# Kernel optimization log

Hardware: AMD Instinct MI355X
Metric: run time of the kernel (lower is better)

## Reference

```python
import jax, jax.numpy as jnp
import numpy as np

# Poincare ball hyperbolic multi-head attention (hypll-style HMultiheadAttention)
C = 1.0          # ball curvature
SQRT_C = 1.0
EPS = 1e-7
B, S, E, H = 4, 1024, 512, 8
HD = E // H      # head_dim = 64


def _project_to_ball(u, scale=0.5):
    n = jnp.linalg.norm(u, axis=-1, keepdims=True)
    return u * (scale / (1.0 + n))  # guarantees ||x|| < scale < 1/sqrt(C)


def h_linear(x, z, r):
    """Poincare fully-connected layer (Shimizu et al. HNN++), as in hypll HLinear.
    x: [..., n] points in the ball, z: [n, m] weight directions, r: [m] bias."""
    x2 = jnp.sum(x * x, -1, keepdims=True)
    lam = 2.0 / jnp.maximum(1.0 - C * x2, EPS)          # conformal factor lambda_x
    zn = jnp.maximum(jnp.linalg.norm(z, axis=0), EPS)    # [m]
    xz = x @ z                                           # [..., m]
    two_cr = 2.0 * SQRT_C * r
    v = (2.0 * zn / SQRT_C) * jnp.arcsinh(
        SQRT_C * lam * xz / zn * jnp.cosh(two_cr) - (lam - 1.0) * jnp.sinh(two_cr)
    )
    v2 = jnp.sum(v * v, -1, keepdims=True)
    return v / (1.0 + jnp.sqrt(1.0 + C * v2))            # map back into the ball


def _split_heads(x):
    b, s, e = x.shape
    return x.reshape(b, s, H, HD).transpose(0, 2, 1, 3)  # [B,H,S,hd]; matches split(dim=-1)


def _h_attention(q, k, v):
    # similarity = -poincare_dist(q, k), pairwise via the arccosh closed form
    # (avoids materializing a [B,H,Sq,Sk,hd] mobius_add tensor)
    q2 = jnp.sum(q * q, -1)[..., :, None]                # [B,H,Sq,1]
    k2 = jnp.sum(k * k, -1)[..., None, :]                # [B,H,1,Sk]
    qk = jnp.einsum('bhqd,bhkd->bhqk', q, k)
    diff2 = jnp.maximum(q2 + k2 - 2.0 * qk, 0.0)
    denom = jnp.maximum((1.0 - C * q2) * (1.0 - C * k2), EPS)
    arg = 1.0 + 2.0 * C * diff2 / denom
    dist = jnp.arccosh(jnp.maximum(arg, 1.0 + EPS)) / SQRT_C
    w = jax.nn.softmax(-dist, axis=-1)                   # attention_activation
    # attention_midpoint: weighted Mobius gyromidpoint then half scalar-mul
    v2 = jnp.sum(v * v, -1)                              # [B,H,Sk]
    lam = 2.0 / jnp.maximum(1.0 - C * v2, EPS)
    num = jnp.einsum('bhqk,bhkd->bhqd', w * lam[..., None, :], v)
    den = jnp.einsum('bhqk,bhk->bhq', w, lam - 1.0)[..., None]
    m_bar = num / jnp.where(jnp.abs(den) < EPS, EPS, den)
    mn = jnp.maximum(jnp.linalg.norm(m_bar, axis=-1, keepdims=True), EPS)
    t = jnp.minimum(SQRT_C * mn, 1.0 - 1e-6)
    return jnp.tanh(0.5 * jnp.arctanh(t)) * m_bar / (SQRT_C * mn)  # (1/2) mobius-scalar-mul


def setup_inputs() -> dict:
    key = jax.random.key(0)
    ks = jax.random.split(key, 9)
    query = _project_to_ball(jax.random.normal(ks[0], (B, S, E), jnp.float32))
    key_t = _project_to_ball(jax.random.normal(ks[1], (B, S, E), jnp.float32))
    value = _project_to_ball(jax.random.normal(ks[2], (B, S, E), jnp.float32))
    scale = E ** -0.5
    zq = jax.random.normal(ks[3], (E, E), jnp.float32) * scale
    zk = jax.random.normal(ks[4], (E, E), jnp.float32) * scale
    zv = jax.random.normal(ks[5], (E, E), jnp.float32) * scale
    rq = jax.random.normal(ks[6], (E,), jnp.float32) * 0.01
    rk = jax.random.normal(ks[7], (E,), jnp.float32) * 0.01
    rv = jax.random.normal(ks[8], (E,), jnp.float32) * 0.01
    return {"query": query, "key": key_t, "value": value,
            "zq": zq, "rq": rq, "zk": zk, "rk": rk, "zv": zv, "rv": rv}


def reference(query, key, value, zq, rq, zk, rk, zv, rv):
    pq = h_linear(query, zq, rq)
    pk = h_linear(key, zk, rk)
    pv = h_linear(value, zv, rv)
    q, k, v = _split_heads(pq), _split_heads(pk), _split_heads(pv)
    out = _h_attention(q, k, v)                          # [B,H,S,hd]
    return out.transpose(0, 2, 1, 3).reshape(B, S, E)    # manifold.cat over heads
```

## Files before the change

kernel.cpp:

```cpp
#include <hip/hip_runtime.h>
#include <math.h>

#define EPSf 1e-7f
typedef unsigned short u16;
typedef __attribute__((ext_vector_type(8))) short bf16x8;
typedef __attribute__((ext_vector_type(4))) float f32x4;

__device__ __forceinline__ float bf2f(u16 u) {
  union { unsigned int i; float f; } x; x.i = ((unsigned int)u) << 16; return x.f;
}
__device__ __forceinline__ u16 f2bf(float f) {
  union { float f; unsigned int i; } x; x.f = f;
  unsigned int r = x.i + 0x7fffu + ((x.i >> 16) & 1u);
  return (u16)(r >> 16);
}
__device__ __forceinline__ void gll16(const void* g, void* l) {
  __builtin_amdgcn_global_load_lds((__attribute__((address_space(1))) void*)(g),
                                   (__attribute__((address_space(3))) void*)(l),
                                   16, 0, 0);
}

__global__ __launch_bounds__(256) void split_x(
    const float* __restrict__ xq, const float* __restrict__ xk, const float* __restrict__ xv,
    u16* __restrict__ Xh, u16* __restrict__ Xl,
    float* __restrict__ Xn, float* __restrict__ Vn, float* __restrict__ Zn) {
  if (blockIdx.x == 0) {
    #pragma unroll
    for (int j = 0; j < 6; ++j) Zn[threadIdx.x + 256 * j] = 0.f;
  }
  const int gr = blockIdx.x * 2 + (threadIdx.x >> 7);
  const int mat = gr >> 12, row = gr & 4095;
  const float* X = (mat == 0) ? xq : (mat == 1) ? xk : xv;
  const int f4 = threadIdx.x & 127;
  float4 x = ((const float4*)(X + (size_t)row * 512))[f4];
  u16 h0 = f2bf(x.x), h1 = f2bf(x.y), h2 = f2bf(x.z), h3 = f2bf(x.w);
  u16 l0 = f2bf(x.x - bf2f(h0)), l1 = f2bf(x.y - bf2f(h1));
  u16 l2 = f2bf(x.z - bf2f(h2)), l3 = f2bf(x.w - bf2f(h3));
  ((ushort4*)(Xh + (size_t)gr * 512))[f4] = make_ushort4(h0, h1, h2, h3);
  ((ushort4*)(Xl + (size_t)gr * 512))[f4] = make_ushort4(l0, l1, l2, l3);
  float a = fmaf(x.x, x.x, fmaf(x.y, x.y, fmaf(x.z, x.z, x.w * x.w)));
  a += __shfl_xor(a, 1);  a += __shfl_xor(a, 2);  a += __shfl_xor(a, 4);
  a += __shfl_xor(a, 8);  a += __shfl_xor(a, 16); a += __shfl_xor(a, 32);
  __shared__ float red[4];
  if ((threadIdx.x & 63) == 0) red[threadIdx.x >> 6] = a;
  __syncthreads();
  if (threadIdx.x == 0)   { Xn[gr] = red[0] + red[1]; Vn[gr] = 0.f; }
  if (threadIdx.x == 128) { Xn[gr] = red[2] + red[3]; Vn[gr] = 0.f; }
}

__global__ __launch_bounds__(256) void split_z(
    const float* __restrict__ zq, const float* __restrict__ zk, const float* __restrict__ zv,
    u16* __restrict__ ZhT, u16* __restrict__ ZlT, float* __restrict__ Zn) {
  const int idx = blockIdx.x;
  const int mat = idx >> 6;
  const int cg = (idx >> 3) & 7, kt = idx & 7;
  const int c0 = cg * 64;
  const float* Z = (mat == 0) ? zq : (mat == 1) ? zk : zv;
  __shared__ float tile[64][68];
  const int t = threadIdx.x;
  {
    int kl = t >> 2;
    const float* src = Z + (size_t)(kt * 64 + kl) * 512 + c0 + (t & 3) * 16;
    #pragma unroll
    for (int j = 0; j < 4; ++j) {
      float4 v = *(const float4*)(src + 4 * j);
      *(float4*)&tile[kl][(t & 3) * 16 + 4 * j] = v;
    }
  }
  __syncthreads();
  const int cl = t >> 2, kg4 = t & 3;
  const size_t zo = (size_t)mat * 512 * 512;
  float csum = 0.f;
  #pragma unroll
  for (int jj = 0; jj < 4; ++jj) {
    u16 hb[4], lb[4];
    #pragma unroll
    for (int qq = 0; qq < 4; ++qq) {
      float zval = tile[kg4 * 16 + jj * 4 + qq][cl];
      csum = fmaf(zval, zval, csum);
      u16 hh = f2bf(zval);
      hb[qq] = hh;
      lb[qq] = f2bf(zval - bf2f(hh));
    }
    size_t o = zo + (size_t)(c0 + cl) * 512 + kt * 64 + kg4 * 16 + jj * 4;
    *(ushort4*)(ZhT + o) = make_ushort4(hb[0], hb[1], hb[2], hb[3]);
    *(ushort4*)(ZlT + o) = make_ushort4(lb[0], lb[1], lb[2], lb[3]);
  }
  csum += __shfl_xor(csum, 1);
  csum += __shfl_xor(csum, 2);
  if (kg4 == 0) atomicAdd(&Zn[mat * 512 + c0 + cl], csum);
}

__global__ __launch_bounds__(256) void proj_gemm(
    const u16* __restrict__ Xh, const u16* __restrict__ Xl,
    const u16* __restrict__ ZhT, const u16* __restrict__ ZlT,
    const float* __restrict__ Xn, const float* __restrict__ Zn,
    const float* __restrict__ rq, const float* __restrict__ rk, const float* __restrict__ rv,
    float* __restrict__ Vtmp, float* __restrict__ Vn) {
  const int m0 = blockIdx.x * 64;
  const int n0 = blockIdx.y * 128;
  const int mat = blockIdx.z;
  const size_t xoff = (size_t)mat * 4096 * 512;
  const size_t zoff = (size_t)mat * 512 * 512;
  const int t = threadIdx.x, wv = t >> 6, lane = t & 63;
  const int l15 = lane & 15, quad = lane >> 4;
  const int wm = wv >> 1, wn = wv & 1;

  __shared__ __align__(16) u16 SM[12288];
  __shared__ float lams[64], lam1s[64], wmxs[128], wmys[128], wmzs[128];

  if (t < 64) {
    float x2 = Xn[mat * 4096 + m0 + t];
    float lam = 2.f / fmaxf(1.f - x2, EPSf);
    lams[t] = lam; lam1s[t] = lam - 1.f;
  }
  if (t < 128) {
    float zn = fmaxf(sqrtf(Zn[mat * 512 + n0 + t]), EPSf);
    const float* R = (mat == 0) ? rq : (mat == 1) ? rk : rv;
    float tr = 2.f * R[n0 + t];
    float e = expf(tr), ei = 1.f / e;
    wmxs[t] = 0.5f * (e + ei) / zn;
    wmys[t] = 0.5f * (e - ei);
    wmzs[t] = 2.f * zn;
  }

  f32x4 acc[2][4];
  #pragma unroll
  for (int i = 0; i < 2; ++i)
    #pragma unroll
    for (int j = 0; j < 4; ++j) acc[i][j] = (f32x4){0.f, 0.f, 0.f, 0.f};

  const u16* gs[6];
  u16* ld[6];
  #pragma unroll
  for (int ci = 0; ci < 6; ++ci) {
    int c = wv + 4 * ci;
    const u16* arr; int row0, lo;
    if (c < 4)       { arr = Xh + xoff;  row0 = m0 + 16 * c;        lo = c * 512; }
    else if (c < 8)  { arr = Xl + xoff;  row0 = m0 + 16 * (c - 4);  lo = 2048 + (c - 4) * 512; }
    else if (c < 16) { arr = ZhT + zoff; row0 = n0 + 16 * (c - 8);  lo = 4096 + (c - 8) * 512; }
    else             { arr = ZlT + zoff; row0 = n0 + 16 * (c - 16); lo = 8192 + (c - 16) * 512; }
    gs[ci] = arr + (size_t)(row0 + (lane >> 2)) * 512 + (lane & 3) * 8;
    ld[ci] = SM + lo;
  }

  for (int k0 = 0; k0 < 512; k0 += 32) {
    __syncthreads();
    #pragma unroll
    for (int ci = 0; ci < 6; ++ci) gll16(gs[ci] + k0, ld[ci]);
    __syncthreads();
    bf16x8 ah[2], al[2], bh_[4], bl_[4];
    #pragma unroll
    for (int i = 0; i < 2; ++i) {
      int ra = wm * 32 + i * 16 + l15;
      ah[i] = *(const bf16x8*)&SM[ra * 32 + quad * 8];
      al[i] = *(const bf16x8*)&SM[2048 + ra * 32 + quad * 8];
    }
    #pragma unroll
    for (int j = 0; j < 4; ++j) {
      int rb = wn * 64 + j * 16 + l15;
      bh_[j] = *(const bf16x8*)&SM[4096 + rb * 32 + quad * 8];
      bl_[j] = *(const bf16x8*)&SM[8192 + rb * 32 + quad * 8];
    }
    #pragma unroll
    for (int i = 0; i < 2; ++i)
      #pragma unroll
      for (int j = 0; j < 4; ++j) {
        acc[i][j] = __builtin_amdgcn_mfma_f32_16x16x32_bf16(ah[i], bh_[j], acc[i][j], 0, 0, 0);
        acc[i][j] = __builtin_amdgcn_mfma_f32_16x16x32_bf16(ah[i], bl_[j], acc[i][j], 0, 0, 0);
        acc[i][j] = __builtin_amdgcn_mfma_f32_16x16x32_bf16(al[i], bh_[j], acc[i][j], 0, 0, 0);
      }
  }

  #pragma unroll
  for (int i = 0; i < 2; ++i) {
    float rsum[4] = {0.f, 0.f, 0.f, 0.f};
    #pragma unroll
    for (int j = 0; j < 4; ++j) {
      int nl = wn * 64 + j * 16 + l15;
      float wx = wmxs[nl], wy = wmys[nl], wz = wmzs[nl];
      #pragma unroll
      for (int r = 0; r < 4; ++r) {
        int ml = wm * 32 + i * 16 + quad * 4 + r;
        float tt = lams[ml] * acc[i][j][r] * wx - lam1s[ml] * wy;
        float v = wz * logf(tt + sqrtf(fmaf(tt, tt, 1.f)));
        Vtmp[xoff + (size_t)(m0 + ml) * 512 + (n0 + nl)] = v;
        rsum[r] = fmaf(v, v, rsum[r]);
      }
    }
    #pragma unroll
    for (int r = 0; r < 4; ++r) {
      rsum[r] += __shfl_xor(rsum[r], 1);
      rsum[r] += __shfl_xor(rsum[r], 2);
      rsum[r] += __shfl_xor(rsum[r], 4);
      rsum[r] += __shfl_xor(rsum[r], 8);
    }
    if (l15 == 0) {
      #pragma unroll
      for (int r = 0; r < 4; ++r)
        atomicAdd(&Vn[mat * 4096 + m0 + wm * 32 + i * 16 + quad * 4 + r], rsum[r]);
    }
  }
}

__global__ __launch_bounds__(256) void pack(
    const float* __restrict__ Vtmp, const float* __restrict__ Vn,
    u16* __restrict__ Qh, u16* __restrict__ Kh, u16* __restrict__ VTb,
    float* __restrict__ q2a, float* __restrict__ aqa, float4* __restrict__ ksc) {
  __shared__ u16 tile[64][72];
  __shared__ float lams[64];
  const int t = threadIdx.x;
  if (blockIdx.x < 256) {
    const int mat = blockIdx.x >> 7;
    const int rb = blockIdx.x & 127;
    const int r = t >> 3, h = t & 7;
    const int row = rb * 32 + r;
    const size_t gr = (size_t)mat * 4096 + row;
    const float sc = 1.f / (1.f + sqrtf(1.f + Vn[gr]));
    const float* src = Vtmp + gr * 512 + h * 64;
    const int b = row >> 10, s = row & 1023;
    u16* dst = (mat ? Kh : Qh) + ((size_t)(b * 8 + h) * 1024 + s) * 64;
    float nrm = 0.f;
    #pragma unroll
    for (int j = 0; j < 16; ++j) {
      float4 x = *(const float4*)(src + 4 * j);
      u16 u0 = f2bf(x.x * sc), u1 = f2bf(x.y * sc), u2 = f2bf(x.z * sc), u3 = f2bf(x.w * sc);
      *(ushort4*)(dst + 4 * j) = make_ushort4(u0, u1, u2, u3);
      float f0 = bf2f(u0), f1 = bf2f(u1), f2 = bf2f(u2), f3 = bf2f(u3);
      nrm += f0 * f0 + f1 * f1 + f2 * f2 + f3 * f3;
    }
    const size_t so = (size_t)(b * 8 + h) * 1024 + s;
    if (mat == 0) { q2a[so] = nrm; aqa[so] = 1.f / fmaxf(1.f - nrm, EPSf); }
    else {
      float2 kk = make_float2(nrm, 2.f / fmaxf(1.f - nrm, EPSf));
      *(float2*)&ksc[so] = kk;
    }
  } else {
    const int idx = blockIdx.x - 256;
    const int bh = idx >> 4, st = idx & 15;
    const int b = bh >> 3, h = bh & 7;
    {
      const int s = t >> 2, dg = t & 3;
      const size_t gr = (size_t)2 * 4096 + b * 1024 + st * 64 + s;
      const float sc = 1.f / (1.f + sqrtf(1.f + Vn[gr]));
      const float* src = Vtmp + gr * 512 + h * 64 + dg * 16;
      float nrm = 0.f;
      #pragma unroll
      for (int j = 0; j < 4; ++j) {
        float4 x = *(const float4*)(src + 4 * j);
        u16 u0 = f2bf(x.x * sc), u1 = f2bf(x.y * sc), u2 = f2bf(x.z * sc), u3 = f2bf(x.w * sc);
        *(ushort4*)&tile[s][dg * 16 + 4 * j] = make_ushort4(u0, u1, u2, u3);
        float f0 = bf2f(u0), f1 = bf2f(u1), f2 = bf2f(u2), f3 = bf2f(u3);
        nrm += f0 * f0 + f1 * f1 + f2 * f2 + f3 * f3;
      }
      nrm += __shfl_xor(nrm, 1);
      nrm += __shfl_xor(nrm, 2);
      if (dg == 0) {
        float lam = 2.f / fmaxf(1.f - nrm, EPSf);
        lams[s] = lam;
        ((float*)&ksc[(size_t)bh * 1024 + st * 64 + s])[3] = lam - 1.f;
      }
    }
    __syncthreads();
    const int d = t >> 2, sg = t & 3;
    u16 ob[16];
    #pragma unroll
    for (int j = 0; j < 16; ++j) {
      int ss = sg * 16 + j;
      ob[j] = f2bf(bf2f(tile[ss][d]) * lams[ss]);
    }
    u16* dst = VTb + ((size_t)bh * 64 + d) * 1024 + st * 64 + sg * 16;
    #pragma unroll
    for (int j = 0; j < 4; ++j)
      *(ushort4*)(dst + 4 * j) = make_ushort4(ob[4 * j], ob[4 * j + 1], ob[4 * j + 2], ob[4 * j + 3]);
  }
}

__global__ __launch_bounds__(256) void attn(
    const u16* __restrict__ Qh, const u16* __restrict__ Kh, const u16* __restrict__ VTb,
    const float* __restrict__ q2a, const float* __restrict__ aqa,
    const float4* __restrict__ ksc, float* __restrict__ out) {
  const int bh = blockIdx.y;
  const int b = bh >> 3, h = bh & 7;
  const int q0 = blockIdx.x * 32;
  const int t = threadIdx.x, wv = t >> 6, lane = t & 63;
  const int l15 = lane & 15, quad = lane >> 4;
  const int qh = wv >> 1, kh = wv & 1;

  __shared__ __align__(16) u16 Qs[32 * 72];
  __shared__ __align__(16) u16 Ks[64 * 72];
  __shared__ __align__(16) u16 VsT[64 * 72];
  __shared__ __align__(16) u16 Ws[4 * 16 * 36];
  __shared__ float dens[64];
  __shared__ __align__(16) float nums[2][16][68];

  {
    int row = t >> 3, g = t & 7;
    float4 v = *(const float4*)(Qh + ((size_t)bh * 1024 + q0 + row) * 64 + g * 8);
    *(float4*)&Qs[row * 72 + g * 8] = v;
  }
  float q2r[4], aqr[4];
  #pragma unroll
  for (int r = 0; r < 4; ++r) {
    int qi = bh * 1024 + q0 + qh * 16 + quad * 4 + r;
    q2r[r] = q2a[qi];
    aqr[r] = aqa[qi];
  }
  __syncthreads();
  const bf16x8 qf0 = *(const bf16x8*)&Qs[(qh * 16 + l15) * 72 + quad * 8];
  const bf16x8 qf1 = *(const bf16x8*)&Qs[(qh * 16 + l15) * 72 + 32 + quad * 8];

  f32x4 num[4];
  #pragma unroll
  for (int i = 0; i < 4; ++i) num[i] = (f32x4){0.f, 0.f, 0.f, 0.f};
  float denp[4] = {0.f, 0.f, 0.f, 0.f};

  for (int kt = 0; kt < 16; ++kt) {
    __syncthreads();
    {
      int row = t >> 3, g = t & 7;
      #pragma unroll
      for (int p = 0; p < 2; ++p) {
        int rr = row + 32 * p;
        float4 kv = *(const float4*)(Kh + ((size_t)bh * 1024 + kt * 64 + rr) * 64 + g * 8);
        *(float4*)&Ks[rr * 72 + g * 8] = kv;
        float4 vvv = *(const float4*)(VTb + ((size_t)bh * 64 + rr) * 1024 + kt * 64 + g * 8);
        *(float4*)&VsT[rr * 72 + g * 8] = vvv;
      }
    }
    __syncthreads();

    f32x4 s0 = (f32x4){0.f, 0.f, 0.f, 0.f};
    f32x4 s1 = (f32x4){0.f, 0.f, 0.f, 0.f};
    {
      const bf16x8 ka0 = *(const bf16x8*)&Ks[(kh * 32 + l15) * 72 + quad * 8];
      const bf16x8 ka1 = *(const bf16x8*)&Ks[(kh * 32 + l15) * 72 + 32 + quad * 8];
      const bf16x8 kb0 = *(const bf16x8*)&Ks[(kh * 32 + 16 + l15) * 72 + quad * 8];
      const bf16x8 kb1 = *(const bf16x8*)&Ks[(kh * 32 + 16 + l15) * 72 + 32 + quad * 8];
      s0 = __builtin_amdgcn_mfma_f32_16x16x32_bf16(qf0, ka0, s0, 0, 0, 0);
      s0 = __builtin_amdgcn_mfma_f32_16x16x32_bf16(qf1, ka1, s0, 0, 0, 0);
      s1 = __builtin_amdgcn_mfma_f32_16x16x32_bf16(qf0, kb0, s1, 0, 0, 0);
      s1 = __builtin_amdgcn_mfma_f32_16x16x32_bf16(qf1, kb1, s1, 0, 0, 0);
    }
    #pragma unroll
    for (int tn = 0; tn < 2; ++tn) {
      float4 kv = ksc[(size_t)bh * 1024 + kt * 64 + kh * 32 + tn * 16 + l15];
      float k2 = kv.x, ck = kv.y, l1f = kv.w;
      f32x4 s = tn ? s1 : s0;
      #pragma unroll
      for (int r = 0; r < 4; ++r) {
        float d2 = fmaxf(fmaf(-2.f, s[r], q2r[r] + k2), 0.f);
        float u = fmaxf(d2 * ck * aqr[r], EPSf);
        float w = (1.f + u) - sqrtf(u * (u + 2.f));
        u16 wb = f2bf(w);
        denp[r] = fmaf(bf2f(wb), l1f, denp[r]);
        Ws[wv * 576 + (quad * 4 + r) * 36 + tn * 16 + l15] = wb;
      }
    }
    const bf16x8 wf = *(const bf16x8*)&Ws[wv * 576 + l15 * 36 + quad * 8];
    #pragma unroll
    for (int tm = 0; tm < 4; ++tm) {
      const bf16x8 vf = *(const bf16x8*)&VsT[(tm * 16 + l15) * 72 + kh * 32 + quad * 8];
      num[tm] = __builtin_amdgcn_mfma_f32_16x16x32_bf16(vf, wf, num[tm], 0, 0, 0);
    }
  }

  #pragma unroll
  for (int r = 0; r < 4; ++r) {
    denp[r] += __shfl_xor(denp[r], 1);
    denp[r] += __shfl_xor(denp[r], 2);
    denp[r] += __shfl_xor(denp[r], 4);
    denp[r] += __shfl_xor(denp[r], 8);
  }
  if (l15 == 0) {
    #pragma unroll
    for (int r = 0; r < 4; ++r) dens[wv * 16 + quad * 4 + r] = denp[r];
  }
  if (kh == 1) {
    #pragma unroll
    for (int tm = 0; tm < 4; ++tm)
      *(float4*)&nums[qh][l15][tm * 16 + quad * 4] =
          make_float4(num[tm][0], num[tm][1], num[tm][2], num[tm][3]);
  }
  __syncthreads();
  if (kh == 0) {
    #pragma unroll
    for (int tm = 0; tm < 4; ++tm) {
      float4 o = *(const float4*)&nums[qh][l15][tm * 16 + quad * 4];
      num[tm][0] += o.x; num[tm][1] += o.y; num[tm][2] += o.z; num[tm][3] += o.w;
    }
    float den = dens[qh * 32 + l15] + dens[qh * 32 + 16 + l15];
    den = (fabsf(den) < EPSf) ? EPSf : den;
    float inv = 1.f / den;
    float mv[4][4];
    float p = 0.f;
    #pragma unroll
    for (int tm = 0; tm < 4; ++tm)
      #pragma unroll
      for (int r = 0; r < 4; ++r) {
        float m = num[tm][r] * inv;
        mv[tm][r] = m;
        p = fmaf(m, m, p);
      }
    p += __shfl_xor(p, 16);
    p += __shfl_xor(p, 32);
    float mn = sqrtf(p);
    float mnc = fmaxf(mn, EPSf);
    float tt2 = fminf(mnc, 1.f - 1e-6f);
    float scale = tt2 / ((1.f + sqrtf(fmaxf(1.f - tt2 * tt2, 0.f))) * mnc);
    const size_t qg = (size_t)b * 1024 + q0 + qh * 16 + l15;
    #pragma unroll
    for (int tm = 0; tm < 4; ++tm) {
      float4 o = make_float4(mv[tm][0] * scale, mv[tm][1] * scale,
                             mv[tm][2] * scale, mv[tm][3] * scale);
      *(float4*)(out + qg * 512 + h * 64 + tm * 16 + quad * 4) = o;
    }
  }
}

extern "C" void kernel_launch(void* const* d_in, const int* in_sizes, int n_in,
                              void* d_out, int out_size, void* d_ws, size_t ws_size,
                              hipStream_t stream) {
  (void)in_sizes; (void)n_in; (void)out_size; (void)ws_size;
  const float* q  = (const float*)d_in[0];
  const float* k  = (const float*)d_in[1];
  const float* v  = (const float*)d_in[2];
  const float* zq = (const float*)d_in[3];
  const float* rq = (const float*)d_in[4];
  const float* zk = (const float*)d_in[5];
  const float* rk = (const float*)d_in[6];
  const float* zv = (const float*)d_in[7];
  const float* rv = (const float*)d_in[8];

  unsigned char* ws = (unsigned char*)d_ws;
  u16*   Xh   = (u16*)(ws + 0);
  u16*   Xl   = (u16*)(ws + 12582912);
  u16*   ZhT  = (u16*)(ws + 25165824);
  u16*   ZlT  = (u16*)(ws + 26738688);
  float* Vtmp = (float*)(ws + 28311552);
  float* Xn   = (float*)(ws + 53477376);
  float* Vn   = (float*)(ws + 53526528);
  float* Zn   = (float*)(ws + 53575680);
  u16*   Qh   = (u16*)(ws + 0);
  u16*   Kh   = (u16*)(ws + 4194304);
  u16*   VTb  = (u16*)(ws + 8388608);
  float* q2a  = (float*)(ws + 12582912);
  float* aqa  = (float*)(ws + 12713984);
  float4* ksc = (float4*)(ws + 12845056);

  split_x<<<6144, 256, 0, stream>>>(q, k, v, Xh, Xl, Xn, Vn, Zn);
  split_z<<<192, 256, 0, stream>>>(zq, zk, zv, ZhT, ZlT, Zn);
  proj_gemm<<<dim3(64, 4, 3), 256, 0, stream>>>(Xh, Xl, ZhT, ZlT, Xn, Zn, rq, rk, rv, Vtmp, Vn);
  pack<<<768, 256, 0, stream>>>(Vtmp, Vn, Qh, Kh, VTb, q2a, aqa, ksc);
  attn<<<dim3(32, 32), 256, 0, stream>>>(Qh, Kh, VTb, q2a, aqa, ksc, (float*)d_out);
}
```

Before: 182.7 us.

## Restructure attention kernel: register-resident K/V fragments with prefetch, 64-query tiles

The attention kernel now processes 64 queries per block, with the key range split between warp pairs by interleaved tiles. K and V fragments are loaded straight from global memory into registers, and the next K tile is prefetched, so the shared-memory staging and the per-tile block barriers go away. The score MFMA operands are swapped so per-key scalars line up with rows, and the bf16 weights are packed two at a time. The grid is halved and swapped to bh-major so blocks for the same head run close together for L2 reuse. In exchange, register pressure rises, which occupancy is bounded by a launch_bounds hint.

```diff
diff --git a/kernel.cpp b/kernel.cpp
--- a/kernel.cpp
+++ b/kernel.cpp
@@ -1,4 +1,5 @@
 #include <hip/hip_runtime.h>
+#include <hip/hip_bf16.h>
 #include <math.h>
 
 #define EPSf 1e-7f
@@ -276,144 +277,168 @@
   }
 }
 
-__global__ __launch_bounds__(256) void attn(
+__global__ __launch_bounds__(256, 2) void attn(
     const u16* __restrict__ Qh, const u16* __restrict__ Kh, const u16* __restrict__ VTb,
     const float* __restrict__ q2a, const float* __restrict__ aqa,
     const float4* __restrict__ ksc, float* __restrict__ out) {
-  const int bh = blockIdx.y;
+  const int bh = blockIdx.x;
   const int b = bh >> 3, h = bh & 7;
-  const int q0 = blockIdx.x * 32;
+  const int q0 = blockIdx.y * 64;
   const int t = threadIdx.x, wv = t >> 6, lane = t & 63;
   const int l15 = lane & 15, quad = lane >> 4;
-  const int qh = wv >> 1, kh = wv & 1;
-
-  __shared__ __align__(16) u16 Qs[32 * 72];
-  __shared__ __align__(16) u16 Ks[64 * 72];
-  __shared__ __align__(16) u16 VsT[64 * 72];
-  __shared__ __align__(16) u16 Ws[4 * 16 * 36];
-  __shared__ float dens[64];
-  __shared__ __align__(16) float nums[2][16][68];
-
-  {
-    int row = t >> 3, g = t & 7;
-    float4 v = *(const float4*)(Qh + ((size_t)bh * 1024 + q0 + row) * 64 + g * 8);
-    *(float4*)&Qs[row * 72 + g * 8] = v;
-  }
-  float q2r[4], aqr[4];
-  #pragma unroll
-  for (int r = 0; r < 4; ++r) {
-    int qi = bh * 1024 + q0 + qh * 16 + quad * 4 + r;
-    q2r[r] = q2a[qi];
-    aqr[r] = aqa[qi];
-  }
-  __syncthreads();
-  const bf16x8 qf0 = *(const bf16x8*)&Qs[(qh * 16 + l15) * 72 + quad * 8];
-  const bf16x8 qf1 = *(const bf16x8*)&Qs[(qh * 16 + l15) * 72 + 32 + quad * 8];
-
-  f32x4 num[4];
-  #pragma unroll
-  for (int i = 0; i < 4; ++i) num[i] = (f32x4){0.f, 0.f, 0.f, 0.f};
-  float denp[4] = {0.f, 0.f, 0.f, 0.f};
-
-  for (int kt = 0; kt < 16; ++kt) {
-    __syncthreads();
-    {
-      int row = t >> 3, g = t & 7;
-      #pragma unroll
-      for (int p = 0; p < 2; ++p) {
-        int rr = row + 32 * p;
-        float4 kv = *(const float4*)(Kh + ((size_t)bh * 1024 + kt * 64 + rr) * 64 + g * 8);
-        *(float4*)&Ks[rr * 72 + g * 8] = kv;
-        float4 vvv = *(const float4*)(VTb + ((size_t)bh * 64 + rr) * 1024 + kt * 64 + g * 8);
-        *(float4*)&VsT[rr * 72 + g * 8] = vvv;
-      }
-    }
-    __syncthreads();
-
-    f32x4 s0 = (f32x4){0.f, 0.f, 0.f, 0.f};
-    f32x4 s1 = (f32x4){0.f, 0.f, 0.f, 0.f};
-    {
-      const bf16x8 ka0 = *(const bf16x8*)&Ks[(kh * 32 + l15) * 72 + quad * 8];
-      const bf16x8 ka1 = *(const bf16x8*)&Ks[(kh * 32 + l15) * 72 + 32 + quad * 8];
-      const bf16x8 kb0 = *(const bf16x8*)&Ks[(kh * 32 + 16 + l15) * 72 + quad * 8];
-      const bf16x8 kb1 = *(const bf16x8*)&Ks[(kh * 32 + 16 + l15) * 72 + 32 + quad * 8];
-      s0 = __builtin_amdgcn_mfma_f32_16x16x32_bf16(qf0, ka0, s0, 0, 0, 0);
-      s0 = __builtin_amdgcn_mfma_f32_16x16x32_bf16(qf1, ka1, s0, 0, 0, 0);
-      s1 = __builtin_amdgcn_mfma_f32_16x16x32_bf16(qf0, kb0, s1, 0, 0, 0);
-      s1 = __builtin_amdgcn_mfma_f32_16x16x32_bf16(qf1, kb1, s1, 0, 0, 0);
-    }
-    #pragma unroll
-    for (int tn = 0; tn < 2; ++tn) {
-      float4 kv = ksc[(size_t)bh * 1024 + kt * 64 + kh * 32 + tn * 16 + l15];
-      float k2 = kv.x, ck = kv.y, l1f = kv.w;
-      f32x4 s = tn ? s1 : s0;
-      #pragma unroll
-      for (int r = 0; r < 4; ++r) {
-        float d2 = fmaxf(fmaf(-2.f, s[r], q2r[r] + k2), 0.f);
-        float u = fmaxf(d2 * ck * aqr[r], EPSf);
-        float w = (1.f + u) - sqrtf(u * (u + 2.f));
-        u16 wb = f2bf(w);
-        denp[r] = fmaf(bf2f(wb), l1f, denp[r]);
-        Ws[wv * 576 + (quad * 4 + r) * 36 + tn * 16 + l15] = wb;
-      }
-    }
-    const bf16x8 wf = *(const bf16x8*)&Ws[wv * 576 + l15 * 36 + quad * 8];
-    #pragma unroll
-    for (int tm = 0; tm < 4; ++tm) {
-      const bf16x8 vf = *(const bf16x8*)&VsT[(tm * 16 + l15) * 72 + kh * 32 + quad * 8];
-      num[tm] = __builtin_amdgcn_mfma_f32_16x16x32_bf16(vf, wf, num[tm], 0, 0, 0);
-    }
-  }
-
-  #pragma unroll
-  for (int r = 0; r < 4; ++r) {
-    denp[r] += __shfl_xor(denp[r], 1);
-    denp[r] += __shfl_xor(denp[r], 2);
-    denp[r] += __shfl_xor(denp[r], 4);
-    denp[r] += __shfl_xor(denp[r], 8);
-  }
-  if (l15 == 0) {
-    #pragma unroll
-    for (int r = 0; r < 4; ++r) dens[wv * 16 + quad * 4 + r] = denp[r];
+  const int qh = wv & 1, kh = wv >> 1;
+
+  __shared__ __align__(16) u16 Ws[4][32 * 72];
+  __shared__ float k2s[4][64], cks[4][64], l1s[4][64];
+  __shared__ __align__(16) float nums[2][32][68];
+  __shared__ float dens[2][32];
+
+  const size_t qkoff = (size_t)bh * 65536;
+
+  bf16x8 qf[2][2];
+  float q2r[2], aqr[2];
+  #pragma unroll
+  for (int qs = 0; qs < 2; ++qs) {
+    int qrow = q0 + qh * 32 + qs * 16 + l15;
+    const u16* qp = Qh + qkoff + (size_t)qrow * 64 + quad * 8;
+    qf[qs][0] = *(const bf16x8*)qp;
+    qf[qs][1] = *(const bf16x8*)(qp + 32);
+    q2r[qs] = q2a[bh * 1024 + qrow];
+    aqr[qs] = aqa[bh * 1024 + qrow];
+  }
+
+  f32x4 num[2][4];
+  #pragma unroll
+  for (int qs = 0; qs < 2; ++qs)
+    #pragma unroll
+    for (int tm = 0; tm < 4; ++tm) num[qs][tm] = (f32x4){0.f, 0.f, 0.f, 0.f};
+  float denp[2] = {0.f, 0.f};
+
+  bf16x8 kcur[8];
+  #pragma unroll
+  for (int tn = 0; tn < 4; ++tn)
+    #pragma unroll
+    for (int ks = 0; ks < 2; ++ks)
+      kcur[tn * 2 + ks] = *(const bf16x8*)(Kh + qkoff +
+          (size_t)(kh * 64 + tn * 16 + l15) * 64 + ks * 32 + quad * 8);
+  float4 scur = ksc[bh * 1024 + kh * 64 + lane];
+
+  #pragma unroll 2
+  for (int i = 0; i < 8; ++i) {
+    const int ktc = kh + 2 * i;
+    const int kti = (i < 7) ? ktc + 2 : ktc;
+    bf16x8 knxt[8];
+    #pragma unroll
+    for (int tn = 0; tn < 4; ++tn)
+      #pragma unroll
+      for (int ks = 0; ks < 2; ++ks)
+        knxt[tn * 2 + ks] = *(const bf16x8*)(Kh + qkoff +
+            (size_t)(kti * 64 + tn * 16 + l15) * 64 + ks * 32 + quad * 8);
+    float4 snxt = ksc[bh * 1024 + kti * 64 + lane];
+    bf16x8 vf[8];
+    #pragma unroll
+    for (int tm = 0; tm < 4; ++tm)
+      #pragma unroll
+      for (int ks = 0; ks < 2; ++ks)
+        vf[tm * 2 + ks] = *(const bf16x8*)(VTb + qkoff +
+            (size_t)(tm * 16 + l15) * 1024 + ktc * 64 + ks * 32 + quad * 8);
+    k2s[wv][lane] = scur.x;
+    cks[wv][lane] = scur.y;
+    l1s[wv][lane] = scur.w;
+
+    #pragma unroll
+    for (int tn = 0; tn < 4; ++tn) {
+      const float4 k2v = *(const float4*)&k2s[wv][tn * 16 + quad * 4];
+      const float4 ckv = *(const float4*)&cks[wv][tn * 16 + quad * 4];
+      const float4 l1v = *(const float4*)&l1s[wv][tn * 16 + quad * 4];
+      #pragma unroll
+      for (int qs = 0; qs < 2; ++qs) {
+        f32x4 s = (f32x4){0.f, 0.f, 0.f, 0.f};
+        s = __builtin_amdgcn_mfma_f32_16x16x32_bf16(kcur[tn * 2 + 0], qf[qs][0], s, 0, 0, 0);
+        s = __builtin_amdgcn_mfma_f32_16x16x32_bf16(kcur[tn * 2 + 1], qf[qs][1], s, 0, 0, 0);
+        unsigned up[2];
+        #pragma unroll
+        for (int pr = 0; pr < 2; ++pr) {
+          float w2[2];
+          #pragma unroll
+          for (int e = 0; e < 2; ++e) {
+            const int r = pr * 2 + e;
+            float d2 = fmaxf(fmaf(-2.f, s[r], q2r[qs] + ((const float*)&k2v)[r]), 0.f);
+            float u = fmaxf(d2 * ((const float*)&ckv)[r] * aqr[qs], EPSf);
+            w2[e] = (1.f + u) - sqrtf(fmaf(u, u, u + u));
+          }
+          union { __hip_bfloat162 h2; unsigned u; } cv;
+          cv.h2 = __float22bfloat162_rn(make_float2(w2[0], w2[1]));
+          up[pr] = cv.u;
+          float wlo = __uint_as_float(cv.u << 16);
+          float whi = __uint_as_float(cv.u & 0xffff0000u);
+          denp[qs] = fmaf(wlo, ((const float*)&l1v)[pr * 2 + 0], denp[qs]);
+          denp[qs] = fmaf(whi, ((const float*)&l1v)[pr * 2 + 1], denp[qs]);
+        }
+        *(uint2*)&Ws[wv][(qs * 16 + l15) * 72 + tn * 16 + quad * 4] = make_uint2(up[0], up[1]);
+      }
+    }
+    #pragma unroll
+    for (int qs = 0; qs < 2; ++qs)
+      #pragma unroll
+      for (int ks = 0; ks < 2; ++ks) {
+        const bf16x8 wf = *(const bf16x8*)&Ws[wv][(qs * 16 + l15) * 72 + ks * 32 + quad * 8];
+        #pragma unroll
+        for (int tm = 0; tm < 4; ++tm)
+          num[qs][tm] = __builtin_amdgcn_mfma_f32_16x16x32_bf16(vf[tm * 2 + ks], wf, num[qs][tm], 0, 0, 0);
+      }
+    #pragma unroll
+    for (int j = 0; j < 8; ++j) kcur[j] = knxt[j];
+    scur = snxt;
+  }
+
+  #pragma unroll
+  for (int qs = 0; qs < 2; ++qs) {
+    denp[qs] += __shfl_xor(denp[qs], 16);
+    denp[qs] += __shfl_xor(denp[qs], 32);
   }
   if (kh == 1) {
     #pragma unroll
-    for (int tm = 0; tm < 4; ++tm)
-      *(float4*)&nums[qh][l15][tm * 16 + quad * 4] =
-          make_float4(num[tm][0], num[tm][1], num[tm][2], num[tm][3]);
+    for (int qs = 0; qs < 2; ++qs) {
+      #pragma unroll
+      for (int tm = 0; tm < 4; ++tm)
+        *(float4*)&nums[qh][qs * 16 + l15][tm * 16 + quad * 4] =
+            make_float4(num[qs][tm][0], num[qs][tm][1], num[qs][tm][2], num[qs][tm][3]);
+      if (quad == 0) dens[qh][qs * 16 + l15] = denp[qs];
+    }
   }
   __syncthreads();
   if (kh == 0) {
     #pragma unroll
-    for (int tm = 0; tm < 4; ++tm) {
-      float4 o = *(const float4*)&nums[qh][l15][tm * 16 + quad * 4];
-      num[tm][0] += o.x; num[tm][1] += o.y; num[tm][2] += o.z; num[tm][3] += o.w;
-    }
-    float den = dens[qh * 32 + l15] + dens[qh * 32 + 16 + l15];
-    den = (fabsf(den) < EPSf) ? EPSf : den;
-    float inv = 1.f / den;
-    float mv[4][4];
-    float p = 0.f;
-    #pragma unroll
-    for (int tm = 0; tm < 4; ++tm)
-      #pragma unroll
-      for (int r = 0; r < 4; ++r) {
-        float m = num[tm][r] * inv;
-        mv[tm][r] = m;
-        p = fmaf(m, m, p);
-      }
-    p += __shfl_xor(p, 16);
-    p += __shfl_xor(p, 32);
-    float mn = sqrtf(p);
-    float mnc = fmaxf(mn, EPSf);
-    float tt2 = fminf(mnc, 1.f - 1e-6f);
-    float scale = tt2 / ((1.f + sqrtf(fmaxf(1.f - tt2 * tt2, 0.f))) * mnc);
-    const size_t qg = (size_t)b * 1024 + q0 + qh * 16 + l15;
-    #pragma unroll
-    for (int tm = 0; tm < 4; ++tm) {
-      float4 o = make_float4(mv[tm][0] * scale, mv[tm][1] * scale,
-                             mv[tm][2] * scale, mv[tm][3] * scale);
-      *(float4*)(out + qg * 512 + h * 64 + tm * 16 + quad * 4) = o;
+    for (int qs = 0; qs < 2; ++qs) {
+      float den = denp[qs] + dens[qh][qs * 16 + l15];
+      den = (fabsf(den) < EPSf) ? EPSf : den;
+      float inv = 1.f / den;
+      float mv[4][4];
+      float p = 0.f;
+      #pragma unroll
+      for (int tm = 0; tm < 4; ++tm) {
+        float4 o = *(const float4*)&nums[qh][qs * 16 + l15][tm * 16 + quad * 4];
+        mv[tm][0] = (num[qs][tm][0] + o.x) * inv;
+        mv[tm][1] = (num[qs][tm][1] + o.y) * inv;
+        mv[tm][2] = (num[qs][tm][2] + o.z) * inv;
+        mv[tm][3] = (num[qs][tm][3] + o.w) * inv;
+        p = fmaf(mv[tm][0], mv[tm][0], p); p = fmaf(mv[tm][1], mv[tm][1], p);
+        p = fmaf(mv[tm][2], mv[tm][2], p); p = fmaf(mv[tm][3], mv[tm][3], p);
+      }
+      p += __shfl_xor(p, 16);
+      p += __shfl_xor(p, 32);
+      float mn = sqrtf(p);
+      float mnc = fmaxf(mn, EPSf);
+      float tt2 = fminf(mnc, 1.f - 1e-6f);
+      float scale = tt2 / ((1.f + sqrtf(fmaxf(1.f - tt2 * tt2, 0.f))) * mnc);
+      const size_t qg = (size_t)b * 1024 + q0 + qh * 32 + qs * 16 + l15;
+      #pragma unroll
+      for (int tm = 0; tm < 4; ++tm) {
+        float4 o = make_float4(mv[tm][0] * scale, mv[tm][1] * scale,
+                               mv[tm][2] * scale, mv[tm][3] * scale);
+        *(float4*)(out + qg * 512 + h * 64 + tm * 16 + quad * 4) = o;
+      }
     }
   }
 }
@@ -452,5 +477,5 @@
   split_z<<<192, 256, 0, stream>>>(zq, zk, zv, ZhT, ZlT, Zn);
   proj_gemm<<<dim3(64, 4, 3), 256, 0, stream>>>(Xh, Xl, ZhT, ZlT, Xn, Zn, rq, rk, rv, Vtmp, Vn);
   pack<<<768, 256, 0, stream>>>(Vtmp, Vn, Qh, Kh, VTb, q2a, aqa, ksc);
-  attn<<<dim3(32, 32), 256, 0, stream>>>(Qh, Kh, VTb, q2a, aqa, ksc, (float*)d_out);
-}
+  attn<<<dim3(32, 16), 256, 0, stream>>>(Qh, Kh, VTb, q2a, aqa, ksc, (float*)d_out);
+}
```

Measured after the change: 177.3 us. 2.9% less time.
